# Kernel optimization log

Measured on AMD Instinct MI355X. Metric: run time of the kernel, lower is better.

## Reference

```python
import jax, jax.numpy as jnp
import numpy as np

N = 100000   # nodes of target type
N1 = 80000   # nodes of second type
D = 128      # raw feature dim
H = 64       # hidden dim
C = 16       # n_classes
G = 3        # number of graphs (metapaths)
E = 1000000  # edges per graph
K = 20       # neighbors per node for NS branch
LP_LAYERS = 3


def setup_inputs() -> dict:
    key = jax.random.key(0)
    ks = jax.random.split(key, 24)
    f = lambda i, shape: jax.random.normal(ks[i], shape, dtype=jnp.float32)
    feats0 = f(0, (N, D))
    feats1 = f(1, (N1, D))
    W0 = f(2, (D, H)) * 0.05
    b0 = jnp.zeros((H,), jnp.float32)
    W1 = f(3, (D, H)) * 0.05
    b1 = jnp.zeros((H,), jnp.float32)
    Wp = f(4, (D, H)) * 0.05
    Wcls = f(5, (H, C)) * 0.05
    bcls = jnp.zeros((C,), jnp.float32)
    alpha = f(6, (N, 1)) * 0.1
    attention = f(7, (N, G, 1))
    y = jax.random.randint(ks[8], (N,), 0, C)
    labels_one_hot = jax.nn.one_hot(y, C, dtype=jnp.float32)
    byte_idx_train = jax.random.bernoulli(ks[9], 0.3, (N, 1))
    label_init = jnp.full((N, C), 1.0 / C, jnp.float32)
    nei_idx = jax.random.randint(ks[10], (N, K), 0, N1, dtype=jnp.int32)
    src0 = jax.random.randint(ks[11], (E,), 0, N, dtype=jnp.int32)
    dst0 = jax.random.randint(ks[12], (E,), 0, N, dtype=jnp.int32)
    src1 = jax.random.randint(ks[13], (E,), 0, N, dtype=jnp.int32)
    dst1 = jax.random.randint(ks[14], (E,), 0, N, dtype=jnp.int32)
    src2 = jax.random.randint(ks[15], (E,), 0, N, dtype=jnp.int32)
    dst2 = jax.random.randint(ks[16], (E,), 0, N, dtype=jnp.int32)
    return dict(feats0=feats0, feats1=feats1, W0=W0, b0=b0, W1=W1, b1=b1,
                Wp=Wp, Wcls=Wcls, bcls=bcls, alpha=alpha, attention=attention,
                labels_one_hot=labels_one_hot, label_init=label_init,
                byte_idx_train=byte_idx_train, nei_idx=nei_idx,
                src0=src0, dst0=dst0, src1=src1, dst1=dst1, src2=src2, dst2=dst2)


def _propagate(fp, h, src, dst, n):
    # edge attention: dot-product score of projected feats, softmax per dst
    s = jnp.sum(fp[src] * fp[dst], axis=-1) / np.sqrt(fp.shape[-1])   # [E]
    m = jax.ops.segment_max(s, dst, num_segments=n)                   # [N]
    e = jnp.exp(s - jnp.where(jnp.isfinite(m), m, 0.0)[dst])          # [E]
    denom = jax.ops.segment_sum(e, dst, num_segments=n)               # [N]
    att = e / (denom[dst] + 1e-16)                                    # [E]
    return jax.ops.segment_sum(att[:, None] * h[src], dst, num_segments=n)


def reference(feats0, feats1, W0, b0, W1, b1, Wp, Wcls, bcls, alpha, attention,
              labels_one_hot, label_init, byte_idx_train, nei_idx,
              src0, dst0, src1, dst1, src2, dst2):
    n = label_init.shape[0]
    masked = byte_idx_train.astype(jnp.float32)          # [N,1]
    masked_label = 1.0 - masked                          # (~mask).float()
    masked_onehot = labels_one_hot * masked              # clamp train labels

    fp = feats0 @ Wp                                     # shared projected feats [N,H]
    h_prime = []
    for src, dst in ((src0, dst0), (src1, dst1), (src2, dst2)):
        h = label_init
        for _ in range(LP_LAYERS):
            h = _propagate(fp, h, src, dst, n)
            h = h * masked_label + masked_onehot
        h_prime.append(h)
    x = jnp.stack(h_prime, axis=-1)                      # [N, C, G]
    att_g = jax.nn.softmax(attention, axis=1)            # [N, G, 1]
    logits_lp = jnp.matmul(x, att_g).squeeze(-1)         # [N, C]

    # NS_ec branch: per-type projection + neighbor-mean aggregation + classifier
    h0 = feats0 @ W0 + b0                                # [N, H]
    h1 = feats1 @ W1 + b1                                # [N1, H]
    z = h0 + jnp.mean(h1[nei_idx], axis=1)               # [N, H]
    logits_ns = z @ Wcls + bcls                          # [N, C]

    gate = jax.nn.sigmoid(alpha)
    logits = gate * logits_lp + jax.nn.sigmoid(-alpha) * logits_ns
    return logits, logits_lp, logits_ns
```

## Files before the change

### kernel.cpp

```cpp
#include <hip/hip_runtime.h>
#include <stdint.h>
#include <stddef.h>

__device__ __forceinline__ float bl(unsigned u){ return __uint_as_float(u << 16); }
__device__ __forceinline__ float bh(unsigned u){ return __uint_as_float(u & 0xffff0000u); }
__device__ __forceinline__ unsigned short f2bf(float f){
    unsigned u = __float_as_uint(f);
    unsigned r = (u + 0x7fffu + ((u >> 16) & 1u)) >> 16;
    return (unsigned short)r;
}
__device__ __forceinline__ float dec15(unsigned e15){
    return __uint_as_float((e15 + (112u << 10)) << 13);
}
__device__ __forceinline__ float get_mask(const void* p, unsigned flags, int i){
    if((flags & 1u) == 0) return ((const int*)p)[i] ? 1.0f : 0.0f;
    if(flags & 2u)        return ((const float*)p)[i];
    return ((const unsigned char*)p)[i] ? 1.0f : 0.0f;
}

__global__ __launch_bounds__(256) void prep_kernel(
    const float* __restrict__ W0, const float* __restrict__ b0,
    const float* __restrict__ W1, const float* __restrict__ b1,
    const float* __restrict__ Wcls, const float* __restrict__ bcls,
    float* __restrict__ W0c, float* __restrict__ W1c,
    float* __restrict__ b0c, float* __restrict__ b1c,
    const unsigned char* __restrict__ mp, int n,
    const unsigned* __restrict__ li, long li_n, unsigned* __restrict__ flags,
    int* __restrict__ deg, int n3)
{
    int t = threadIdx.x;
    if(blockIdx.x == 0){
        for(int i = t; i < 2048; i += 256){
            int d = i >> 4, c = i & 15;
            float s0 = 0.f, s1 = 0.f;
            for(int k = 0; k < 64; k++){
                float wc = Wcls[k*16 + c];
                s0 += W0[d*64 + k]*wc;
                s1 += W1[d*64 + k]*wc;
            }
            W0c[i] = s0; W1c[i] = s1;
        }
        if(t < 16){
            float s0 = 0.f, s1 = 0.f;
            for(int k = 0; k < 64; k++){
                float wc = Wcls[k*16 + t];
                s0 += b0[k]*wc; s1 += b1[k]*wc;
            }
            b0c[t] = s0 + bcls[t];
            b1c[t] = s1;
        }
    } else {
        long i = (long)(blockIdx.x - 1)*256 + t;
        if(i < n3) deg[i] = 0;
        unsigned f = 0;
        if(i < n){
            unsigned char b = mp[i];
            if((i & 3) && b) f |= 1u;
            if(b == 0x3Fu)   f |= 2u;
        }
        if(i < li_n){
            if(li[i] != li[0]) f |= 4u;
        }
        if(f) atomicOr(flags, f);
    }
}

__global__ __launch_bounds__(256) void proj_fused0(
    const float* __restrict__ X, const float* __restrict__ Wp,
    const float* __restrict__ W0c, const float* __restrict__ b0c,
    unsigned short* __restrict__ fph, float* __restrict__ h0c, int rows)
{
    __shared__ float Wl[128*64];
    __shared__ float Wcl[128*16];
    __shared__ float ftile[32*128];
    int t = threadIdx.x;
    for(int i = t; i < 2048; i += 256) ((float4*)Wl)[i]  = ((const float4*)Wp)[i];
    for(int i = t; i < 512;  i += 256) ((float4*)Wcl)[i] = ((const float4*)W0c)[i];
    int c4 = (t & 15)*4;
    int col16 = t & 15;
    int r2 = (t >> 4)*2;
    float bc = b0c[col16];
    for(long base = (long)blockIdx.x*32; base < rows; base += (long)gridDim.x*32){
        int nr = min(32, (int)(rows - base));
        __syncthreads();
        for(int i = t; i < nr*32; i += 256){
            int r = i >> 5, q = i & 31;
            ((float4*)ftile)[r*32 + q] = ((const float4*)X)[(base + r)*32 + q];
        }
        __syncthreads();
        float a00=0,a01=0,a02=0,a03=0, a10=0,a11=0,a12=0,a13=0;
        float c0 = bc, c1 = bc;
        #pragma unroll 4
        for(int k = 0; k < 128; k++){
            float4 w = *((const float4*)(Wl + k*64 + c4));
            float wc = Wcl[k*16 + col16];
            float x0 = ftile[r2*128 + k];
            float x1 = ftile[(r2+1)*128 + k];
            a00 += x0*w.x; a01 += x0*w.y; a02 += x0*w.z; a03 += x0*w.w; c0 += x0*wc;
            a10 += x1*w.x; a11 += x1*w.y; a12 += x1*w.z; a13 += x1*w.w; c1 += x1*wc;
        }
        if(r2 < nr){
            ushort4 o; o.x=f2bf(a00); o.y=f2bf(a01); o.z=f2bf(a02); o.w=f2bf(a03);
            *((ushort4*)(fph + (base + r2)*64 + c4)) = o;
            h0c[(base + r2)*16 + col16] = c0;
        }
        if(r2 + 1 < nr){
            ushort4 o; o.x=f2bf(a10); o.y=f2bf(a11); o.z=f2bf(a12); o.w=f2bf(a13);
            *((ushort4*)(fph + (base + r2 + 1)*64 + c4)) = o;
            h0c[(base + r2 + 1)*16 + col16] = c1;
        }
    }
}

__global__ __launch_bounds__(256) void proj16_kernel(
    const float* __restrict__ X, const float* __restrict__ Wc,
    const float* __restrict__ biasc, unsigned short* __restrict__ Y, int rows)
{
    __shared__ float Wcl[128*16];
    __shared__ float ftile[64*128];
    int t = threadIdx.x;
    for(int i = t; i < 512; i += 256) ((float4*)Wcl)[i] = ((const float4*)Wc)[i];
    int col = t & 15;
    int r4 = (t >> 4)*4;
    float bc = biasc[col];
    long base = (long)blockIdx.x*64;
    if(base >= rows) return;
    int nr = min(64, (int)(rows - base));
    __syncthreads();
    for(int i = t; i < nr*32; i += 256){
        int r = i >> 5, q = i & 31;
        ((float4*)ftile)[r*32 + q] = ((const float4*)X)[(base + r)*32 + q];
    }
    __syncthreads();
    float acc0 = bc, acc1 = bc, acc2 = bc, acc3 = bc;
    #pragma unroll 4
    for(int k = 0; k < 128; k++){
        float wc = Wcl[k*16 + col];
        acc0 += ftile[(r4+0)*128 + k]*wc;
        acc1 += ftile[(r4+1)*128 + k]*wc;
        acc2 += ftile[(r4+2)*128 + k]*wc;
        acc3 += ftile[(r4+3)*128 + k]*wc;
    }
    if(r4+0 < nr) Y[(base + r4 + 0)*16 + col] = f2bf(acc0);
    if(r4+1 < nr) Y[(base + r4 + 1)*16 + col] = f2bf(acc1);
    if(r4+2 < nr) Y[(base + r4 + 2)*16 + col] = f2bf(acc2);
    if(r4+3 < nr) Y[(base + r4 + 3)*16 + col] = f2bf(acc3);
}

__global__ __launch_bounds__(256) void count_rank_kernel(
    const int* __restrict__ dst0, const int* __restrict__ dst1, const int* __restrict__ dst2,
    int* __restrict__ deg, int* __restrict__ rank, int n, int eg)
{
    long tid = (long)blockIdx.x*blockDim.x + threadIdx.x;
    if(tid < 3L*eg){
        int g = (int)(tid / eg);
        int e = (int)(tid - (long)g*eg);
        const int* dp = g==0 ? dst0 : (g==1 ? dst1 : dst2);
        int r = atomicAdd(&deg[(long)g*n + dp[e]], 1);
        __builtin_nontemporal_store(r, rank + tid);
    }
}

__global__ __launch_bounds__(256) void scanA_kernel(const int* __restrict__ deg,
                                                    int* __restrict__ incl,
                                                    int* __restrict__ bsum, int n3)
{
    __shared__ int sh[256];
    int t = threadIdx.x;
    long base = (long)blockIdx.x*1024 + t*4;
    int v0=0,v1=0,v2=0,v3=0;
    if(base   < n3) v0 = deg[base];
    if(base+1 < n3) v1 = deg[base+1];
    if(base+2 < n3) v2 = deg[base+2];
    if(base+3 < n3) v3 = deg[base+3];
    int tot = v0+v1+v2+v3;
    sh[t] = tot;
    __syncthreads();
    for(int ofs = 1; ofs < 256; ofs <<= 1){
        int add = (t >= ofs) ? sh[t-ofs] : 0;
        __syncthreads();
        sh[t] += add;
        __syncthreads();
    }
    int pre = sh[t] - tot;
    if(t == 255) bsum[blockIdx.x] = sh[255];
    int s0 = pre+v0, s1 = s0+v1, s2 = s1+v2, s3 = s2+v3;
    if(base   < n3) incl[base]   = s0;
    if(base+1 < n3) incl[base+1] = s1;
    if(base+2 < n3) incl[base+2] = s2;
    if(base+3 < n3) incl[base+3] = s3;
}

__global__ __launch_bounds__(512) void scanB_kernel(int* __restrict__ bsum, int nb)
{
    __shared__ int sh[512];
    int t = threadIdx.x;
    int v = (t < nb) ? bsum[t] : 0;
    sh[t] = v;
    __syncthreads();
    for(int ofs = 1; ofs < 512; ofs <<= 1){
        int add = (t >= ofs) ? sh[t-ofs] : 0;
        __syncthreads();
        sh[t] += add;
        __syncthreads();
    }
    if(t < nb) bsum[t] = sh[t] - v;
}

__global__ __launch_bounds__(256) void scanC_kernel(
    const int* __restrict__ incl, const int* __restrict__ boff,
    int* __restrict__ rowptr, int n3,
    const float* __restrict__ label_init, const float* __restrict__ labels,
    const void* __restrict__ maskp, const unsigned* __restrict__ flags,
    unsigned short* __restrict__ hA, int n)
{
    int i = blockIdx.x*blockDim.x + threadIdx.x;
    if(i >= n3) return;
    int ex = (i == 0) ? 0 : (incl[i-1] + boff[(i-1) >> 10]);
    int en = incl[i] + boff[i >> 10];
    rowptr[i] = ex;
    if(i == n3-1) rowptr[n3] = en;
    unsigned fl = *flags;
    if(!(fl & 4u)){
        int g = i / n;
        int d = i - g*n;
        float mk = get_mask(maskp, fl, d);
        float v = (en > ex) ? label_init[0]*(1.0f - mk) : 0.0f;
        const float4* lb = (const float4*)(labels + (long)d*16);
        ushort4* op = (ushort4*)(hA + (long)i*16);
        #pragma unroll
        for(int q = 0; q < 4; q++){
            float4 l4 = lb[q];
            ushort4 o;
            o.x = f2bf(v + l4.x*mk);
            o.y = f2bf(v + l4.y*mk);
            o.z = f2bf(v + l4.z*mk);
            o.w = f2bf(v + l4.w*mk);
            op[q] = o;
        }
    }
}

__global__ __launch_bounds__(256) void score_scatter_packed(
    const unsigned short* __restrict__ fph,
    const int* __restrict__ src0, const int* __restrict__ dst0,
    const int* __restrict__ src1, const int* __restrict__ dst1,
    const int* __restrict__ src2, const int* __restrict__ dst2,
    const int* __restrict__ rowptr, const int* __restrict__ rank,
    unsigned* __restrict__ rec, int n, int eg)
{
    long tid = (long)blockIdx.x*blockDim.x + threadIdx.x;
    long gid = tid >> 3;
    long tot = 3L*eg;
    long e0 = gid*4;
    if(e0 >= tot) return;
    int l = threadIdx.x & 7;
    const uint4* f4 = (const uint4*)fph;

    int sv[4], dv[4], gv[4], rk[4];
    bool ok[4];
    #pragma unroll
    for(int q = 0; q < 4; q++){
        long e = e0 + q;
        ok[q] = (e < tot);
        long ee = ok[q] ? e : (tot - 1);
        int g = (int)(ee / eg);
        int i = (int)(ee - (long)g*eg);
        const int* sp = g==0 ? src0 : (g==1 ? src1 : src2);
        const int* dp = g==0 ? dst0 : (g==1 ? dst1 : dst2);
        sv[q] = sp[i];
        dv[q] = dp[i];
        gv[q] = g;
        rk[q] = rank[ee];
    }
    uint4 A[4], B[4];
    #pragma unroll
    for(int q = 0; q < 4; q++){
        A[q] = f4[(long)sv[q]*8 + l];
        B[q] = f4[(long)dv[q]*8 + l];
    }
    float p[4];
    #pragma unroll
    for(int q = 0; q < 4; q++){
        float v;
        v  = bl(A[q].x)*bl(B[q].x) + bh(A[q].x)*bh(B[q].x);
        v += bl(A[q].y)*bl(B[q].y) + bh(A[q].y)*bh(B[q].y);
        v += bl(A[q].z)*bl(B[q].z) + bh(A[q].z)*bh(B[q].z);
        v += bl(A[q].w)*bl(B[q].w) + bh(A[q].w)*bh(B[q].w);
        p[q] = v;
    }
    #pragma unroll
    for(int q = 0; q < 4; q++){
        p[q] += __shfl_xor(p[q], 1);
        p[q] += __shfl_xor(p[q], 2);
        p[q] += __shfl_xor(p[q], 4);
    }
    if(l == 0){
        #pragma unroll
        for(int q = 0; q < 4; q++){
            if(ok[q]){
                int pos = rowptr[(long)gv[q]*n + dv[q]] + rk[q];
                float s = fminf(fmaxf(p[q]*0.125f, -10.0f), 10.0f);
                unsigned u = __float_as_uint(__expf(s)) + 0x1000u;
                unsigned e15 = (u >> 13) - (112u << 10);
                unsigned pk = (e15 << 17) | (unsigned)sv[q];
                __builtin_nontemporal_store(pk, rec + pos);
            }
        }
    }
}

__device__ __forceinline__ void prop_row_bf16(
    const unsigned* __restrict__ rec, int beg, int end,
    const unsigned short* __restrict__ hg, int c4,
    float &a0, float &a1, float &a2, float &a3)
{
    float den = 0.f;
    a0 = a1 = a2 = a3 = 0.f;
    int j = beg;
    if((j & 1) && j < end){
        unsigned p = rec[j];
        float e = dec15(p >> 17);
        den += e;
        uint2 hv = *((const uint2*)(hg + (long)(p & 0x1FFFFu)*16 + c4));
        a0 += e*bl(hv.x); a1 += e*bh(hv.x); a2 += e*bl(hv.y); a3 += e*bh(hv.y);
        j++;
    }
    for(; j + 1 < end; j += 2){
        uint2 rr = *((const uint2*)(rec + j));
        float e0 = dec15(rr.x >> 17);
        float e1 = dec15(rr.y >> 17);
        den += e0 + e1;
        uint2 hv0 = *((const uint2*)(hg + (long)(rr.x & 0x1FFFFu)*16 + c4));
        uint2 hv1 = *((const uint2*)(hg + (long)(rr.y & 0x1FFFFu)*16 + c4));
        a0 += e0*bl(hv0.x) + e1*bl(hv1.x);
        a1 += e0*bh(hv0.x) + e1*bh(hv1.x);
        a2 += e0*bl(hv0.y) + e1*bl(hv1.y);
        a3 += e0*bh(hv0.y) + e1*bh(hv1.y);
    }
    if(j < end){
        unsigned p = rec[j];
        float e = dec15(p >> 17);
        den += e;
        uint2 hv = *((const uint2*)(hg + (long)(p & 0x1FFFFu)*16 + c4));
        a0 += e*bl(hv.x); a1 += e*bh(hv.x); a2 += e*bl(hv.y); a3 += e*bh(hv.y);
    }
    float inv = 1.0f/(den + 1e-16f);
    a0 *= inv; a1 *= inv; a2 *= inv; a3 *= inv;
}

__global__ __launch_bounds__(256) void prop1_fallback_kernel(
    const int* __restrict__ rowptr, const unsigned* __restrict__ rec,
    const float* __restrict__ h_in_f32, unsigned short* __restrict__ h_next,
    const float* __restrict__ labels, const void* __restrict__ maskp,
    const unsigned* __restrict__ flags, int n)
{
    unsigned fl = *flags;
    if(!(fl & 4u)) return;
    long tid = (long)blockIdx.x*blockDim.x + threadIdx.x;
    int row = (int)(tid >> 2);
    int c4 = (int)(tid & 3)*4;
    if(row >= 3*n) return;
    int g = row / n;
    int d = row - g*n;
    int beg = rowptr[row], end = rowptr[row+1];
    float a0=0.f, a1=0.f, a2=0.f, a3=0.f, den=0.f;
    for(int j = beg; j < end; j++){
        unsigned p = rec[j];
        float e = dec15(p >> 17);
        den += e;
        float4 hv = *((const float4*)(h_in_f32 + (long)(p & 0x1FFFFu)*16 + c4));
        a0 += e*hv.x; a1 += e*hv.y; a2 += e*hv.z; a3 += e*hv.w;
    }
    float inv = 1.0f/(den + 1e-16f);
    float mk = get_mask(maskp, fl, d);
    float im = (1.0f - mk)*inv;
    float4 lb = *((const float4*)(labels + (long)d*16 + c4));
    ushort4 o;
    o.x = f2bf(a0*im + lb.x*mk);
    o.y = f2bf(a1*im + lb.y*mk);
    o.z = f2bf(a2*im + lb.z*mk);
    o.w = f2bf(a3*im + lb.w*mk);
    *((ushort4*)(h_next + (long)row*16 + c4)) = o;
}

__global__ __launch_bounds__(256) void prop_mid_ns_kernel(
    const int* __restrict__ rowptr, const unsigned* __restrict__ rec,
    const unsigned short* __restrict__ h_in, unsigned short* __restrict__ h_next,
    const float* __restrict__ labels, const void* __restrict__ maskp,
    const unsigned* __restrict__ flags, int n, int nbMid,
    const float* __restrict__ h0c, const unsigned short* __restrict__ h1c,
    const int* __restrict__ nei, float* __restrict__ out, int kk)
{
    int t = threadIdx.x;
    if(blockIdx.x < nbMid){
        long tid = (long)blockIdx.x*256 + t;
        int row = (int)(tid >> 2);
        int c4 = (int)(tid & 3)*4;
        if(row >= 3*n) return;
        int g = row / n;
        int d = row - g*n;
        float a0, a1, a2, a3;
        prop_row_bf16(rec, rowptr[row], rowptr[row+1], h_in + (long)g*n*16, c4,
                      a0, a1, a2, a3);
        unsigned fl = *flags;
        float mk = get_mask(maskp, fl, d);
        float im = 1.0f - mk;
        float4 lb = *((const float4*)(labels + (long)d*16 + c4));
        ushort4 o;
        o.x = f2bf(a0*im + lb.x*mk);
        o.y = f2bf(a1*im + lb.y*mk);
        o.z = f2bf(a2*im + lb.z*mk);
        o.w = f2bf(a3*im + lb.w*mk);
        *((ushort4*)(h_next + (long)row*16 + c4)) = o;
    } else {
        long tid = (long)(blockIdx.x - nbMid)*256 + t;
        int node = (int)(tid >> 2);
        int c4 = (int)(tid & 3)*4;
        if(node >= n) return;
        const int* nrow = nei + (long)node*kk;
        float s0=0.f, s1=0.f, s2=0.f, s3=0.f;
        for(int j = 0; j < kk; j++){
            int nb = nrow[j];
            uint2 hv = *((const uint2*)(h1c + (long)nb*16 + c4));
            s0 += bl(hv.x); s1 += bh(hv.x); s2 += bl(hv.y); s3 += bh(hv.y);
        }
        float invk = 1.0f/(float)kk;
        float4 h0 = *((const float4*)(h0c + (long)node*16 + c4));
        float4 o2;
        o2.x = h0.x + s0*invk; o2.y = h0.y + s1*invk;
        o2.z = h0.z + s2*invk; o2.w = h0.w + s3*invk;
        *((float4*)(out + (long)2*n*16 + (long)node*16 + c4)) = o2;
    }
}

__global__ __launch_bounds__(256) void prop3_ns_kernel(
    const int* __restrict__ rowptr, const unsigned* __restrict__ rec,
    const unsigned short* __restrict__ h_in, const float* __restrict__ labels,
    const void* __restrict__ maskp, const unsigned* __restrict__ flags,
    const float* __restrict__ attn, const float* __restrict__ alpha,
    float* __restrict__ out, int n)
{
    long tid = (long)blockIdx.x*blockDim.x + threadIdx.x;
    int node = (int)(tid >> 2);
    int c4 = (int)(tid & 3)*4;
    if(node >= n) return;
    unsigned fl = *flags;
    float mk = get_mask(maskp, fl, node);
    float im = 1.0f - mk;
    float4 lb = *((const float4*)(labels + (long)node*16 + c4));

    float lp_[3][4];
    #pragma unroll
    for(int g = 0; g < 3; g++){
        int row = g*n + node;
        float a0, a1, a2, a3;
        prop_row_bf16(rec, rowptr[row], rowptr[row+1], h_in + (long)g*n*16, c4,
                      a0, a1, a2, a3);
        lp_[g][0] = a0*im + lb.x*mk;
        lp_[g][1] = a1*im + lb.y*mk;
        lp_[g][2] = a2*im + lb.z*mk;
        lp_[g][3] = a3*im + lb.w*mk;
    }
    float t0 = attn[node*3], t1 = attn[node*3+1], t2 = attn[node*3+2];
    float mx = fmaxf(t0, fmaxf(t1, t2));
    float e0 = __expf(t0-mx), e1 = __expf(t1-mx), e2 = __expf(t2-mx);
    float inv = 1.0f/(e0+e1+e2);
    e0 *= inv; e1 *= inv; e2 *= inv;
    float lp0 = e0*lp_[0][0] + e1*lp_[1][0] + e2*lp_[2][0];
    float lp1 = e0*lp_[0][1] + e1*lp_[1][1] + e2*lp_[2][1];
    float lp2 = e0*lp_[0][2] + e1*lp_[1][2] + e2*lp_[2][2];
    float lp3 = e0*lp_[0][3] + e1*lp_[1][3] + e2*lp_[2][3];

    long gs = (long)n*16;
    long idx = (long)node*16 + c4;
    float4 ns = *((const float4*)(out + 2*gs + idx));
    float al = alpha[node];
    float sg = 1.0f/(1.0f + __expf(-al));
    float isg = 1.0f - sg;
    float4 o0; o0.x = sg*lp0 + isg*ns.x; o0.y = sg*lp1 + isg*ns.y;
               o0.z = sg*lp2 + isg*ns.z; o0.w = sg*lp3 + isg*ns.w;
    float4 o1; o1.x = lp0; o1.y = lp1; o1.z = lp2; o1.w = lp3;
    *((float4*)(out + idx))      = o0;
    *((float4*)(out + gs + idx)) = o1;
}

extern "C" void kernel_launch(void* const* d_in, const int* in_sizes, int n_in,
                              void* d_out, int out_size, void* d_ws, size_t ws_size,
                              hipStream_t stream)
{
    const float* feats0     = (const float*)d_in[0];
    const float* feats1     = (const float*)d_in[1];
    const float* W0         = (const float*)d_in[2];
    const float* b0         = (const float*)d_in[3];
    const float* W1         = (const float*)d_in[4];
    const float* b1         = (const float*)d_in[5];
    const float* Wp         = (const float*)d_in[6];
    const float* Wcls       = (const float*)d_in[7];
    const float* bcls       = (const float*)d_in[8];
    const float* alpha      = (const float*)d_in[9];
    const float* attn       = (const float*)d_in[10];
    const float* labels     = (const float*)d_in[11];
    const float* label_init = (const float*)d_in[12];
    const void*  maskp      = d_in[13];
    const int*   nei        = (const int*)d_in[14];
    const int*   src0       = (const int*)d_in[15];
    const int*   dst0       = (const int*)d_in[16];
    const int*   src1       = (const int*)d_in[17];
    const int*   dst1       = (const int*)d_in[18];
    const int*   src2       = (const int*)d_in[19];
    const int*   dst2       = (const int*)d_in[20];

    const int n  = in_sizes[9];
    const int n1 = in_sizes[1] / 128;
    const int eg = in_sizes[15];
    const int kk = in_sizes[14] / n;
    const int n3 = 3*n;

    char* ws = (char*)d_ws;
    size_t off = 0;
    auto alloc = [&](size_t bytes)->char*{
        char* p = ws + off; off += (bytes + 255) & ~(size_t)255; return p;
    };
    unsigned*       flags  = (unsigned*)      alloc(256);
    unsigned short* fph    = (unsigned short*)alloc((size_t)n*64*2);
    float*          h0c    = (float*)         alloc((size_t)n*16*4);
    unsigned short* h1c    = (unsigned short*)alloc((size_t)n1*16*2);
    float*          W0c    = (float*)         alloc(2048*4);
    float*          W1c    = (float*)         alloc(2048*4);
    float*          b0c    = (float*)         alloc(64);
    float*          b1c    = (float*)         alloc(64);
    int*            deg    = (int*)           alloc((size_t)n3*4);
    int*            bsum   = (int*)           alloc(512*4);
    int*            rowptr = (int*)           alloc(((size_t)n3+1)*4);
    int*            rank   = (int*)           alloc((size_t)3*eg*4);
    unsigned*       rec    = (unsigned*)      alloc((size_t)3*eg*4);
    unsigned short* hA     = (unsigned short*)alloc((size_t)n3*16*2);
    unsigned short* hB     = (unsigned short*)alloc((size_t)n3*16*2);
    int* incl = deg;

    hipMemsetAsync(flags, 0, 4, stream);

    long li_n = (long)n*16;
    {
        unsigned gsz = 1 + (unsigned)((li_n + 255)/256);
        prep_kernel<<<gsz, 256, 0, stream>>>(W0, b0, W1, b1, Wcls, bcls,
                                             W0c, W1c, b0c, b1c,
                                             (const unsigned char*)maskp, n,
                                             (const unsigned*)label_init, li_n, flags,
                                             deg, n3);
    }

    proj_fused0<<<(n+31)/32, 256, 0, stream>>>(feats0, Wp, W0c, b0c, fph, h0c, n);
    proj16_kernel<<<(n1+63)/64, 256, 0, stream>>>(feats1, W1c, b1c, h1c, n1);

    {
        long tot = 3L*eg;
        count_rank_kernel<<<(unsigned)((tot+255)/256), 256, 0, stream>>>(
            dst0, dst1, dst2, deg, rank, n, eg);
    }

    int nb = (n3 + 1023)/1024;
    scanA_kernel<<<nb, 256, 0, stream>>>(deg, incl, bsum, n3);
    scanB_kernel<<<1, 512, 0, stream>>>(bsum, nb);
    scanC_kernel<<<(n3+255)/256, 256, 0, stream>>>(incl, bsum, rowptr, n3,
                                                   label_init, labels, maskp, flags,
                                                   hA, n);

    {
        long groups = (3L*eg + 3)/4;
        long tthreads = groups*8;
        score_scatter_packed<<<(unsigned)((tthreads+255)/256), 256, 0, stream>>>(
            fph, src0,dst0,src1,dst1,src2,dst2, rowptr, rank, rec, n, eg);
    }

    prop1_fallback_kernel<<<(unsigned)(((long)n3*4+255)/256), 256, 0, stream>>>(
        rowptr, rec, label_init, hA, labels, maskp, flags, n);
    {
        int nbMid = (int)(((long)n3*4 + 255)/256);
        int nbNS  = (int)(((long)n*4 + 255)/256);
        prop_mid_ns_kernel<<<nbMid + nbNS, 256, 0, stream>>>(
            rowptr, rec, hA, hB, labels, maskp, flags, n, nbMid,
            h0c, h1c, nei, (float*)d_out, kk);
    }

    prop3_ns_kernel<<<(unsigned)(((long)n*4+255)/256), 256, 0, stream>>>(
        rowptr, rec, hB, labels, maskp, flags, attn, alpha, (float*)d_out, n);
}
```

Baseline: 452.0 us.

## Merge degree-count and projection kernels into one block-specialized launch

The atomic degree-count/rank kernel and the two feature-projection kernels are combined into a single launch where block ranges take on different roles. The atomic-heavy, latency-bound counting can then overlap with the compute- and bandwidth-heavy projection GEMMs, and two launches are saved. The cost is that every block reserves the largest shared memory footprint (56KB), which can lower occupancy for the counting blocks.

```diff
diff --git a/kernel.cpp b/kernel.cpp
--- a/kernel.cpp
+++ b/kernel.cpp
@@ -65,99 +65,98 @@
     }
 }
 
-__global__ __launch_bounds__(256) void proj_fused0(
-    const float* __restrict__ X, const float* __restrict__ Wp,
+__global__ __launch_bounds__(256) void mega_kernel(
+    const int* __restrict__ dst0, const int* __restrict__ dst1, const int* __restrict__ dst2,
+    int* __restrict__ deg, int* __restrict__ rank, int n, int eg, int nbCount,
+    const float* __restrict__ X0, const float* __restrict__ Wp,
     const float* __restrict__ W0c, const float* __restrict__ b0c,
-    unsigned short* __restrict__ fph, float* __restrict__ h0c, int rows)
-{
-    __shared__ float Wl[128*64];
-    __shared__ float Wcl[128*16];
-    __shared__ float ftile[32*128];
+    unsigned short* __restrict__ fph, float* __restrict__ h0c, int rows0, int nbP0,
+    const float* __restrict__ X1, const float* __restrict__ W1c,
+    const float* __restrict__ b1c, unsigned short* __restrict__ h1c, int rows1)
+{
+    __shared__ __align__(16) float smem[14336];
     int t = threadIdx.x;
-    for(int i = t; i < 2048; i += 256) ((float4*)Wl)[i]  = ((const float4*)Wp)[i];
-    for(int i = t; i < 512;  i += 256) ((float4*)Wcl)[i] = ((const float4*)W0c)[i];
-    int c4 = (t & 15)*4;
-    int col16 = t & 15;
-    int r2 = (t >> 4)*2;
-    float bc = b0c[col16];
-    for(long base = (long)blockIdx.x*32; base < rows; base += (long)gridDim.x*32){
-        int nr = min(32, (int)(rows - base));
-        __syncthreads();
-        for(int i = t; i < nr*32; i += 256){
-            int r = i >> 5, q = i & 31;
-            ((float4*)ftile)[r*32 + q] = ((const float4*)X)[(base + r)*32 + q];
-        }
-        __syncthreads();
-        float a00=0,a01=0,a02=0,a03=0, a10=0,a11=0,a12=0,a13=0;
-        float c0 = bc, c1 = bc;
-        #pragma unroll 4
-        for(int k = 0; k < 128; k++){
-            float4 w = *((const float4*)(Wl + k*64 + c4));
-            float wc = Wcl[k*16 + col16];
-            float x0 = ftile[r2*128 + k];
-            float x1 = ftile[(r2+1)*128 + k];
-            a00 += x0*w.x; a01 += x0*w.y; a02 += x0*w.z; a03 += x0*w.w; c0 += x0*wc;
-            a10 += x1*w.x; a11 += x1*w.y; a12 += x1*w.z; a13 += x1*w.w; c1 += x1*wc;
-        }
-        if(r2 < nr){
-            ushort4 o; o.x=f2bf(a00); o.y=f2bf(a01); o.z=f2bf(a02); o.w=f2bf(a03);
-            *((ushort4*)(fph + (base + r2)*64 + c4)) = o;
-            h0c[(base + r2)*16 + col16] = c0;
-        }
-        if(r2 + 1 < nr){
-            ushort4 o; o.x=f2bf(a10); o.y=f2bf(a11); o.z=f2bf(a12); o.w=f2bf(a13);
-            *((ushort4*)(fph + (base + r2 + 1)*64 + c4)) = o;
-            h0c[(base + r2 + 1)*16 + col16] = c1;
-        }
-    }
-}
-
-__global__ __launch_bounds__(256) void proj16_kernel(
-    const float* __restrict__ X, const float* __restrict__ Wc,
-    const float* __restrict__ biasc, unsigned short* __restrict__ Y, int rows)
-{
-    __shared__ float Wcl[128*16];
-    __shared__ float ftile[64*128];
-    int t = threadIdx.x;
-    for(int i = t; i < 512; i += 256) ((float4*)Wcl)[i] = ((const float4*)Wc)[i];
-    int col = t & 15;
-    int r4 = (t >> 4)*4;
-    float bc = biasc[col];
-    long base = (long)blockIdx.x*64;
-    if(base >= rows) return;
-    int nr = min(64, (int)(rows - base));
-    __syncthreads();
-    for(int i = t; i < nr*32; i += 256){
-        int r = i >> 5, q = i & 31;
-        ((float4*)ftile)[r*32 + q] = ((const float4*)X)[(base + r)*32 + q];
-    }
-    __syncthreads();
-    float acc0 = bc, acc1 = bc, acc2 = bc, acc3 = bc;
-    #pragma unroll 4
-    for(int k = 0; k < 128; k++){
-        float wc = Wcl[k*16 + col];
-        acc0 += ftile[(r4+0)*128 + k]*wc;
-        acc1 += ftile[(r4+1)*128 + k]*wc;
-        acc2 += ftile[(r4+2)*128 + k]*wc;
-        acc3 += ftile[(r4+3)*128 + k]*wc;
-    }
-    if(r4+0 < nr) Y[(base + r4 + 0)*16 + col] = f2bf(acc0);
-    if(r4+1 < nr) Y[(base + r4 + 1)*16 + col] = f2bf(acc1);
-    if(r4+2 < nr) Y[(base + r4 + 2)*16 + col] = f2bf(acc2);
-    if(r4+3 < nr) Y[(base + r4 + 3)*16 + col] = f2bf(acc3);
-}
-
-__global__ __launch_bounds__(256) void count_rank_kernel(
-    const int* __restrict__ dst0, const int* __restrict__ dst1, const int* __restrict__ dst2,
-    int* __restrict__ deg, int* __restrict__ rank, int n, int eg)
-{
-    long tid = (long)blockIdx.x*blockDim.x + threadIdx.x;
-    if(tid < 3L*eg){
-        int g = (int)(tid / eg);
-        int e = (int)(tid - (long)g*eg);
-        const int* dp = g==0 ? dst0 : (g==1 ? dst1 : dst2);
-        int r = atomicAdd(&deg[(long)g*n + dp[e]], 1);
-        __builtin_nontemporal_store(r, rank + tid);
+    int b = blockIdx.x;
+    if(b < nbCount){
+        long tid = (long)b*256 + t;
+        if(tid < 3L*eg){
+            int g = (int)(tid / eg);
+            int e = (int)(tid - (long)g*eg);
+            const int* dp = g==0 ? dst0 : (g==1 ? dst1 : dst2);
+            int r = atomicAdd(&deg[(long)g*n + dp[e]], 1);
+            __builtin_nontemporal_store(r, rank + tid);
+        }
+    } else if(b < nbCount + nbP0){
+        float* Wl    = smem;
+        float* Wcl   = smem + 8192;
+        float* ftile = smem + 10240;
+        for(int i = t; i < 2048; i += 256) ((float4*)Wl)[i]  = ((const float4*)Wp)[i];
+        for(int i = t; i < 512;  i += 256) ((float4*)Wcl)[i] = ((const float4*)W0c)[i];
+        int c4 = (t & 15)*4;
+        int col16 = t & 15;
+        int r2 = (t >> 4)*2;
+        float bc = b0c[col16];
+        long base = (long)(b - nbCount)*32;
+        if(base < rows0){
+            int nr = min(32, (int)(rows0 - base));
+            __syncthreads();
+            for(int i = t; i < nr*32; i += 256){
+                int r = i >> 5, q = i & 31;
+                ((float4*)ftile)[r*32 + q] = ((const float4*)X0)[(base + r)*32 + q];
+            }
+            __syncthreads();
+            float a00=0,a01=0,a02=0,a03=0, a10=0,a11=0,a12=0,a13=0;
+            float c0 = bc, c1 = bc;
+            #pragma unroll 4
+            for(int k = 0; k < 128; k++){
+                float4 w = *((const float4*)(Wl + k*64 + c4));
+                float wc = Wcl[k*16 + col16];
+                float x0 = ftile[r2*128 + k];
+                float x1 = ftile[(r2+1)*128 + k];
+                a00 += x0*w.x; a01 += x0*w.y; a02 += x0*w.z; a03 += x0*w.w; c0 += x0*wc;
+                a10 += x1*w.x; a11 += x1*w.y; a12 += x1*w.z; a13 += x1*w.w; c1 += x1*wc;
+            }
+            if(r2 < nr){
+                ushort4 o; o.x=f2bf(a00); o.y=f2bf(a01); o.z=f2bf(a02); o.w=f2bf(a03);
+                *((ushort4*)(fph + (base + r2)*64 + c4)) = o;
+                h0c[(base + r2)*16 + col16] = c0;
+            }
+            if(r2 + 1 < nr){
+                ushort4 o; o.x=f2bf(a10); o.y=f2bf(a11); o.z=f2bf(a12); o.w=f2bf(a13);
+                *((ushort4*)(fph + (base + r2 + 1)*64 + c4)) = o;
+                h0c[(base + r2 + 1)*16 + col16] = c1;
+            }
+        }
+    } else {
+        float* Wcl   = smem;
+        float* ftile = smem + 2048;
+        for(int i = t; i < 512; i += 256) ((float4*)Wcl)[i] = ((const float4*)W1c)[i];
+        int col = t & 15;
+        int r4 = (t >> 4)*4;
+        float bc = b1c[col];
+        long base = (long)(b - nbCount - nbP0)*64;
+        if(base < rows1){
+            int nr = min(64, (int)(rows1 - base));
+            __syncthreads();
+            for(int i = t; i < nr*32; i += 256){
+                int r = i >> 5, q = i & 31;
+                ((float4*)ftile)[r*32 + q] = ((const float4*)X1)[(base + r)*32 + q];
+            }
+            __syncthreads();
+            float acc0 = bc, acc1 = bc, acc2 = bc, acc3 = bc;
+            #pragma unroll 4
+            for(int k = 0; k < 128; k++){
+                float wc = Wcl[k*16 + col];
+                acc0 += ftile[(r4+0)*128 + k]*wc;
+                acc1 += ftile[(r4+1)*128 + k]*wc;
+                acc2 += ftile[(r4+2)*128 + k]*wc;
+                acc3 += ftile[(r4+3)*128 + k]*wc;
+            }
+            if(r4+0 < nr) h1c[(base + r4 + 0)*16 + col] = f2bf(acc0);
+            if(r4+1 < nr) h1c[(base + r4 + 1)*16 + col] = f2bf(acc1);
+            if(r4+2 < nr) h1c[(base + r4 + 2)*16 + col] = f2bf(acc2);
+            if(r4+3 < nr) h1c[(base + r4 + 3)*16 + col] = f2bf(acc3);
+        }
     }
 }
 
@@ -551,13 +550,15 @@
                                              deg, n3);
     }
 
-    proj_fused0<<<(n+31)/32, 256, 0, stream>>>(feats0, Wp, W0c, b0c, fph, h0c, n);
-    proj16_kernel<<<(n1+63)/64, 256, 0, stream>>>(feats1, W1c, b1c, h1c, n1);
-
     {
         long tot = 3L*eg;
-        count_rank_kernel<<<(unsigned)((tot+255)/256), 256, 0, stream>>>(
-            dst0, dst1, dst2, deg, rank, n, eg);
+        int nbCount = (int)((tot + 255)/256);
+        int nbP0    = (n + 31)/32;
+        int nbP16   = (n1 + 63)/64;
+        mega_kernel<<<nbCount + nbP0 + nbP16, 256, 0, stream>>>(
+            dst0, dst1, dst2, deg, rank, n, eg, nbCount,
+            feats0, Wp, W0c, b0c, fph, h0c, n, nbP0,
+            feats1, W1c, b1c, h1c, n1);
     }
 
     int nb = (n3 + 1023)/1024;
```

Measured after the change: 440.8 us, median of 2. 1.03x faster.
